# Kernel tuning notes

Measured on AMD Instinct MI355X. Metric: run time of the kernel, lower is better.

The kernel has to match this reference:

```python
import jax, jax.numpy as jnp
import numpy as np

N_LEVELS = 16
N_FEATS = 2
LOG2_T = 19
TABLE_SIZE = 2 ** LOG2_T
BASE_RES = 16
PER_LEVEL_SCALE = 1.3819
N_PTS = 524288
# per-level grid resolutions (static)
RESOLUTIONS = np.floor(BASE_RES * PER_LEVEL_SCALE ** np.arange(N_LEVELS)).astype(np.float32)
# NGP spatial hash primes for 2D
PRIME0 = np.uint32(1)
PRIME1 = np.uint32(2654435761)
# corner offsets for bilinear interp: (0,0),(0,1),(1,0),(1,1)
CORNER_OFFS = np.array([[0, 0], [0, 1], [1, 0], [1, 1]], dtype=np.uint32)


def setup_inputs() -> dict:
    key = jax.random.key(0)
    k1, k2 = jax.random.split(key)
    pts = jax.random.uniform(k1, (N_PTS, 3), dtype=jnp.float32)  # coords in [0,1]
    # 3 planes x L levels x T entries x F features, small init like NGP (1e-4)
    tables = jax.random.normal(k2, (3, N_LEVELS, TABLE_SIZE, N_FEATS), dtype=jnp.float32) * 1e-4
    return {"pts": pts, "tables": tables}


def _encode_plane(coords, table):
    # coords: [N,2] in [0,1]; table: [L,T,F]
    L, T, F = table.shape
    res = jnp.asarray(RESOLUTIONS)  # [L]
    scaled = coords[None, :, :] * res[:, None, None]  # [L,N,2]
    x0 = jnp.floor(scaled)
    frac = scaled - x0  # [L,N,2]
    x0u = x0.astype(jnp.uint32)
    offs = jnp.asarray(CORNER_OFFS)  # [4,2]
    corners = x0u[:, :, None, :] + offs[None, None, :, :]  # [L,N,4,2]
    # NGP spatial hash with uint32 wraparound, then mod table size
    h = (corners[..., 0] * PRIME0) ^ (corners[..., 1] * PRIME1)  # [L,N,4] uint32
    idx = (h % jnp.uint32(T)).astype(jnp.int32)  # [L,N,4]
    feats = table[jnp.arange(L)[:, None, None], idx]  # [L,N,4,F]
    # bilinear weights: product over dims of frac (offset=1) or 1-frac (offset=0)
    fo = offs.astype(coords.dtype)  # [4,2]
    w = jnp.prod(jnp.where(fo[None, None] > 0, frac[:, :, None, :], 1.0 - frac[:, :, None, :]), axis=-1)  # [L,N,4]
    out = jnp.einsum('lnc,lncf->lnf', w, feats)  # [L,N,F]
    return out.transpose(1, 0, 2).reshape(coords.shape[0], L * F)  # [N, L*F]


def reference(pts, tables):
    # coordinate-pair planes: combinations of (0,1,2) taken 2 at a time
    coo_combs = [(0, 1), (0, 2), (1, 2)]
    interp_space = 1.0
    for ci, comb in enumerate(coo_combs):
        interp_space = interp_space * _encode_plane(pts[:, list(comb)], tables[ci])
    return interp_space  # [N, 32]
```

## Files before the change

kernel.cpp:

```cpp
#include <hip/hip_runtime.h>
#include <stdint.h>


#define NPTS   524288u
#define TSIZE  524288u
#define TMASK  0x7FFFFu
#define PRIME1 2654435761u

__constant__ float c_res[16] = {
    16.f, 22.f, 30.f, 42.f, 58.f, 80.f, 111.f, 153.f,
    212.f, 294.f, 406.f, 561.f, 775.f, 1072.f, 1481.f, 2047.f
};
__constant__ int c_resi[6] = {16, 22, 30, 42, 58, 80};

__constant__ uint8_t c_hmap[32] = {
    15, 31, 47, 14, 30, 46, 13, 29,
    45, 28, 44, 12, 11, 27, 43, 10,
    26, 42,  9, 25, 41,  8, 24, 40,
     7, 23, 39,  6, 22, 38, 255, 255
};

__global__ __launch_bounds__(512) void kplane_lds(
    const float* __restrict__ pts,
    const float2* __restrict__ tab,
    float2* __restrict__ ws)
{
    __shared__ float2 sm[6561];
    const uint32_t b     = blockIdx.x;
    const uint32_t gidx  = b >> 6;
    const uint32_t chunk = b & 63u;
    const uint32_t plane = gidx / 6u;
    const uint32_t lvl   = gidx - plane * 6u;
    const uint32_t g     = plane * 16u + lvl;
    const uint32_t R     = (uint32_t)c_resi[lvl] + 1u;
    const uint32_t E     = R * R;
    const float    res   = c_res[lvl];
    const uint32_t base  = g * TSIZE;
    const uint32_t t     = threadIdx.x;

    for (uint32_t i = t; i < E; i += 512u) {
        const uint32_t cx = i / R;
        const uint32_t cy = i - cx * R;
        sm[i] = tab[base + ((cx ^ (cy * PRIME1)) & TMASK)];
    }
    __syncthreads();

    const uint32_t c0  = (plane == 2u) ? 1u : 0u;
    const uint32_t c1  = (plane == 0u) ? 1u : 2u;
    const uint32_t pt0 = chunk * 8192u + t;

#pragma unroll 4
    for (uint32_t k = 0; k < 16u; ++k) {
        const uint32_t pt = pt0 + k * 512u;
        const float s0 = pts[pt * 3u + c0] * res;
        const float s1 = pts[pt * 3u + c1] * res;
        const float f0 = floorf(s0);
        const float f1 = floorf(s1);
        const float r0 = s0 - f0;
        const float r1 = s1 - f1;
        const uint32_t ci = (uint32_t)f0 * R + (uint32_t)f1;
        const float2 q00 = sm[ci];
        const float2 q01 = sm[ci + 1u];
        const float2 q10 = sm[ci + R];
        const float2 q11 = sm[ci + R + 1u];
        const float w00 = (1.f - r0) * (1.f - r1);
        const float w01 = (1.f - r0) * r1;
        const float w10 = r0 * (1.f - r1);
        const float w11 = r0 * r1;
        ws[g * NPTS + pt] = make_float2(
            w00 * q00.x + w01 * q01.x + w10 * q10.x + w11 * q11.x,
            w00 * q00.y + w01 * q01.y + w10 * q10.y + w11 * q11.y);
    }
}

__global__ __launch_bounds__(256) void kplane_hi(
    const float* __restrict__ pts,
    const float2* __restrict__ tab,
    float2* __restrict__ ws)
{
    const uint32_t b     = blockIdx.x;
    const uint32_t xcd   = b & 7u;
    const uint32_t s     = b >> 3;
    const uint32_t phase = s >> 10;
    const uint32_t chunk = s & 1023u;
    const uint32_t g     = c_hmap[phase * 8u + xcd];
    if (g == 255u) return;
    const uint32_t plane = g >> 4;
    const uint32_t lvl   = g & 15u;
    const float    res   = c_res[lvl];
    const uint32_t c0    = (plane == 2u) ? 1u : 0u;
    const uint32_t c1    = (plane == 0u) ? 1u : 2u;
    const uint32_t base  = g * TSIZE;
    const float4* __restrict__ tab4 = (const float4*)tab;
    const uint32_t b4    = g * (TSIZE / 2u);
    const uint32_t pt0   = chunk * 512u + threadIdx.x;

    float4 P0[2], P1[2];
    float2 Q0[2], Q1[2];
    float  r0[2], r1[2];
    uint32_t sel0[2], sel1[2], oddm[2];

#pragma unroll
    for (int k = 0; k < 2; ++k) {
        const uint32_t pt = pt0 + (uint32_t)k * 256u;
        const float s0 = pts[pt * 3u + c0] * res;
        const float s1 = pts[pt * 3u + c1] * res;
        const float f0 = floorf(s0);
        const float f1 = floorf(s1);
        r0[k] = s0 - f0;
        r1[k] = s1 - f1;
        const uint32_t u0  = (uint32_t)f0;
        const uint32_t hy0 = (uint32_t)f1 * PRIME1;
        const uint32_t hy1 = hy0 + PRIME1;
        const uint32_t i00 = ( u0        ^ hy0) & TMASK;
        const uint32_t i01 = ( u0        ^ hy1) & TMASK;
        const uint32_t i10 = ((u0 + 1u)  ^ hy0) & TMASK;
        const uint32_t i11 = ((u0 + 1u)  ^ hy1) & TMASK;
        sel0[k] = i00 & 1u;
        sel1[k] = i01 & 1u;
        oddm[k] = u0 & 1u;
        P0[k] = tab4[b4 + (i00 >> 1)];
        P1[k] = tab4[b4 + (i01 >> 1)];
        Q0[k] = make_float2(0.f, 0.f);
        Q1[k] = make_float2(0.f, 0.f);
        if (oddm[k]) {
            Q0[k] = tab[base + i10];
            Q1[k] = tab[base + i11];
        }
    }
#pragma unroll
    for (int k = 0; k < 2; ++k) {
        const uint32_t pt = pt0 + (uint32_t)k * 256u;
        const float2 lo0 = make_float2(P0[k].x, P0[k].y);
        const float2 hi0 = make_float2(P0[k].z, P0[k].w);
        const float2 lo1 = make_float2(P1[k].x, P1[k].y);
        const float2 hi1 = make_float2(P1[k].z, P1[k].w);
        const float2 t00 = sel0[k] ? hi0 : lo0;
        const float2 t01 = sel1[k] ? hi1 : lo1;
        const float2 t10 = oddm[k] ? Q0[k] : (sel0[k] ? lo0 : hi0);
        const float2 t11 = oddm[k] ? Q1[k] : (sel1[k] ? lo1 : hi1);
        const float w00 = (1.f - r0[k]) * (1.f - r1[k]);
        const float w01 = (1.f - r0[k]) * r1[k];
        const float w10 = r0[k] * (1.f - r1[k]);
        const float w11 = r0[k] * r1[k];
        ws[g * NPTS + pt] = make_float2(
            w00 * t00.x + w01 * t01.x + w10 * t10.x + w11 * t11.x,
            w00 * t00.y + w01 * t01.y + w10 * t10.y + w11 * t11.y);
    }
}

__global__ __launch_bounds__(256) void kplane_combine(
    const float2* __restrict__ ws,
    float2* __restrict__ out)
{
    __shared__ float2 tile[16][65];
    const uint32_t pt0 = blockIdx.x * 64u;
    const uint32_t t   = threadIdx.x;
    const uint32_t lr  = t >> 6;
    const uint32_t ptl = t & 63u;

#pragma unroll
    for (int k = 0; k < 4; ++k) {
        const uint32_t lvl = (uint32_t)k * 4u + lr;
        const float2 a = ws[( 0u + lvl) * NPTS + pt0 + ptl];
        const float2 b = ws[(16u + lvl) * NPTS + pt0 + ptl];
        const float2 c = ws[(32u + lvl) * NPTS + pt0 + ptl];
        tile[lvl][ptl] = make_float2(a.x * b.x * c.x, a.y * b.y * c.y);
    }
    __syncthreads();
#pragma unroll
    for (int k = 0; k < 4; ++k) {
        const uint32_t e      = t + (uint32_t)k * 256u;
        const uint32_t out_lv = e & 15u;
        const uint32_t out_pt = e >> 4;
        out[(pt0 + out_pt) * 16u + out_lv] = tile[out_lv][out_pt];
    }
}

template <int P, bool FIRST>
__global__ __launch_bounds__(256) void kplane_pass(
    const float* __restrict__ pts,
    const float2* __restrict__ tab,
    float2* __restrict__ ws)
{
    const uint32_t b     = blockIdx.x;
    const uint32_t xcd   = b & 7u;
    const uint32_t s     = b >> 3;
    const uint32_t gi    = s >> 11;
    const uint32_t chunk = s & 2047u;
    const uint32_t lvl   = gi * 8u + xcd;
    const uint32_t pt    = chunk * 256u + threadIdx.x;

    constexpr int c0 = (P == 2) ? 1 : 0;
    constexpr int c1 = (P == 0) ? 1 : 2;

    const float a0  = pts[pt * 3u + c0];
    const float a1  = pts[pt * 3u + c1];
    const float res = c_res[lvl];

    const float s0 = a0 * res;
    const float s1 = a1 * res;
    const float f0 = floorf(s0);
    const float f1 = floorf(s1);
    const float r0 = s0 - f0;
    const float r1 = s1 - f1;
    const uint32_t u0 = (uint32_t)f0;
    const uint32_t hy0  = (uint32_t)f1 * PRIME1;
    const uint32_t hy1  = hy0 + PRIME1;
    const uint32_t base = ((uint32_t)P * 16u + lvl) * TSIZE;

    const float2 t00 = tab[base + (( u0       ^ hy0) & TMASK)];
    const float2 t01 = tab[base + (( u0       ^ hy1) & TMASK)];
    const float2 t10 = tab[base + (((u0 + 1u) ^ hy0) & TMASK)];
    const float2 t11 = tab[base + (((u0 + 1u) ^ hy1) & TMASK)];

    const float w00 = (1.f - r0) * (1.f - r1);
    const float w01 = (1.f - r0) * r1;
    const float w10 = r0 * (1.f - r1);
    const float w11 = r0 * r1;

    const float e0 = w00 * t00.x + w01 * t01.x + w10 * t10.x + w11 * t11.x;
    const float e1 = w00 * t00.y + w01 * t01.y + w10 * t10.y + w11 * t11.y;

    const uint32_t widx = lvl * NPTS + pt;
    if (FIRST) {
        ws[widx] = make_float2(e0, e1);
    } else {
        const float2 prev = ws[widx];
        ws[widx] = make_float2(prev.x * e0, prev.y * e1);
    }
}

__global__ __launch_bounds__(256) void kplane_transpose(
    const float2* __restrict__ ws, float2* __restrict__ out)
{
    const uint32_t tid = blockIdx.x * 256u + threadIdx.x;
    const uint32_t lvl = tid & 15u;
    const uint32_t pt  = tid >> 4;
    out[tid] = ws[lvl * NPTS + pt];
}

extern "C" void kernel_launch(void* const* d_in, const int* in_sizes, int n_in,
                              void* d_out, int out_size, void* d_ws, size_t ws_size,
                              hipStream_t stream) {
    const float*  pts = (const float*)d_in[0];
    const float2* tab = (const float2*)d_in[1];
    float2*       out = (float2*)d_out;

    const size_t wsA = (size_t)48 * NPTS * sizeof(float2);
    const size_t wsB = (size_t)16 * NPTS * sizeof(float2);
    dim3 block256(256u), block512(512u);

    if (ws_size >= wsA) {
        float2* ws = (float2*)d_ws;
        dim3 hgrid(4u * 8u * 1024u);
        hipLaunchKernelGGL(kplane_hi, hgrid, block256, 0, stream, pts, tab, ws);
        dim3 lgrid(18u * 64u);
        hipLaunchKernelGGL(kplane_lds, lgrid, block512, 0, stream, pts, tab, ws);
        dim3 cgrid(NPTS / 64u);
        hipLaunchKernelGGL(kplane_combine, cgrid, block256, 0, stream, ws, out);
    } else if (ws_size >= wsB) {
        float2* ws = (float2*)d_ws;
        dim3 grid(16u * (NPTS / 256u));
        hipLaunchKernelGGL((kplane_pass<0, true >), grid, block256, 0, stream, pts, tab, ws);
        hipLaunchKernelGGL((kplane_pass<1, false>), grid, block256, 0, stream, pts, tab, ws);
        hipLaunchKernelGGL((kplane_pass<2, false>), grid, block256, 0, stream, pts, tab, ws);
        dim3 tgrid((NPTS * 16u) / 256u);
        hipLaunchKernelGGL(kplane_transpose, tgrid, block256, 0, stream, ws, out);
    }
}
```

Measured before the change: 288.2 us.

## Stage levels 6-7 hash tables in LDS via row-split blocks, rebalance hashed kernel

Adds a kplane_mid kernel that handles levels 6 and 7 for all three planes. It splits each level's dense grid into row bands small enough to fit in LDS, and every block filters points to its band before doing bilinear lookups from shared memory. kplane_hi now covers only levels 8-15, with a simpler per-XCD level mapping and four points per thread. This is meant to move gathers for the mid levels from global memory to LDS and to give more latency hiding per thread. The cost is that every mid block reads all points in its chunk and discards most of them, and there is one extra kernel launch.

```diff
diff --git a/kernel.cpp b/kernel.cpp
--- a/kernel.cpp
+++ b/kernel.cpp
@@ -13,12 +13,8 @@
 };
 __constant__ int c_resi[6] = {16, 22, 30, 42, 58, 80};
 
-__constant__ uint8_t c_hmap[32] = {
-    15, 31, 47, 14, 30, 46, 13, 29,
-    45, 28, 44, 12, 11, 27, 43, 10,
-    26, 42,  9, 25, 41,  8, 24, 40,
-     7, 23, 39,  6, 22, 38, 255, 255
-};
+__constant__ uint16_t c_mid_lo[6]  = {0, 56, 0, 39, 78, 117};
+__constant__ uint16_t c_mid_hiX[6] = {56, 112, 39, 78, 117, 154};
 
 __global__ __launch_bounds__(512) void kplane_lds(
     const float* __restrict__ pts,
@@ -73,6 +69,67 @@
     }
 }
 
+__global__ __launch_bounds__(512) void kplane_mid(
+    const float* __restrict__ pts,
+    const float2* __restrict__ tab,
+    float2* __restrict__ ws)
+{
+    __shared__ float2 sm[6400];
+    const uint32_t b     = blockIdx.x;
+    const uint32_t sg    = b >> 5;
+    const uint32_t chunk = b & 31u;
+    const uint32_t plane = sg / 6u;
+    const uint32_t local = sg - plane * 6u;
+    const uint32_t lvl   = (local < 2u) ? 6u : 7u;
+    const uint32_t g     = plane * 16u + lvl;
+    const uint32_t R     = (lvl == 6u) ? 112u : 154u;
+    const uint32_t lo    = c_mid_lo[local];
+    const uint32_t hiX   = c_mid_hiX[local];
+    const uint32_t nrows = ((hiX < R ? hiX : R - 1u) - lo) + 1u;
+    const uint32_t E     = nrows * R;
+    const float    res   = c_res[lvl];
+    const uint32_t base  = g * TSIZE;
+    const uint32_t t     = threadIdx.x;
+
+    for (uint32_t i = t; i < E; i += 512u) {
+        const uint32_t rr = i / R;
+        const uint32_t cy = i - rr * R;
+        const uint32_t cx = lo + rr;
+        sm[i] = tab[base + ((cx ^ (cy * PRIME1)) & TMASK)];
+    }
+    __syncthreads();
+
+    const uint32_t c0  = (plane == 2u) ? 1u : 0u;
+    const uint32_t c1  = (plane == 0u) ? 1u : 2u;
+    const uint32_t pt0 = chunk * 16384u + t;
+
+#pragma unroll 4
+    for (uint32_t k = 0; k < 32u; ++k) {
+        const uint32_t pt = pt0 + k * 512u;
+        const float s0 = pts[pt * 3u + c0] * res;
+        const float s1 = pts[pt * 3u + c1] * res;
+        const float f0 = floorf(s0);
+        const float f1 = floorf(s1);
+        const uint32_t u0 = (uint32_t)f0;
+        if (u0 >= lo && u0 < hiX) {
+            const float r0 = s0 - f0;
+            const float r1 = s1 - f1;
+            const uint32_t ci = (u0 - lo) * R + (uint32_t)f1;
+            const float2 q00 = sm[ci];
+            const float2 q01 = sm[ci + 1u];
+            const float2 q10 = sm[ci + R];
+            const float2 q11 = sm[ci + R + 1u];
+            const float w00 = (1.f - r0) * (1.f - r1);
+            const float w01 = (1.f - r0) * r1;
+            const float w10 = r0 * (1.f - r1);
+            const float w11 = r0 * r1;
+            ws[g * NPTS + pt] = make_float2(
+                w00 * q00.x + w01 * q01.x + w10 * q10.x + w11 * q11.x,
+                w00 * q00.y + w01 * q01.y + w10 * q10.y + w11 * q11.y);
+        }
+    }
+}
+
 __global__ __launch_bounds__(256) void kplane_hi(
     const float* __restrict__ pts,
     const float2* __restrict__ tab,
@@ -81,27 +138,26 @@
     const uint32_t b     = blockIdx.x;
     const uint32_t xcd   = b & 7u;
     const uint32_t s     = b >> 3;
-    const uint32_t phase = s >> 10;
-    const uint32_t chunk = s & 1023u;
-    const uint32_t g     = c_hmap[phase * 8u + xcd];
-    if (g == 255u) return;
-    const uint32_t plane = g >> 4;
-    const uint32_t lvl   = g & 15u;
+    const uint32_t phase = s >> 9;
+    const uint32_t chunk = s & 511u;
+    const uint32_t plane = phase;
+    const uint32_t lvl   = 8u + ((xcd + 3u * phase) & 7u);
+    const uint32_t g     = plane * 16u + lvl;
     const float    res   = c_res[lvl];
     const uint32_t c0    = (plane == 2u) ? 1u : 0u;
     const uint32_t c1    = (plane == 0u) ? 1u : 2u;
     const uint32_t base  = g * TSIZE;
     const float4* __restrict__ tab4 = (const float4*)tab;
     const uint32_t b4    = g * (TSIZE / 2u);
-    const uint32_t pt0   = chunk * 512u + threadIdx.x;
-
-    float4 P0[2], P1[2];
-    float2 Q0[2], Q1[2];
-    float  r0[2], r1[2];
-    uint32_t sel0[2], sel1[2], oddm[2];
+    const uint32_t pt0   = chunk * 1024u + threadIdx.x;
+
+    float4 P0[4], P1[4];
+    float2 Q0[4], Q1[4];
+    float  r0[4], r1[4];
+    uint32_t sel0[4], sel1[4], oddm[4];
 
 #pragma unroll
-    for (int k = 0; k < 2; ++k) {
+    for (int k = 0; k < 4; ++k) {
         const uint32_t pt = pt0 + (uint32_t)k * 256u;
         const float s0 = pts[pt * 3u + c0] * res;
         const float s1 = pts[pt * 3u + c1] * res;
@@ -129,7 +185,7 @@
         }
     }
 #pragma unroll
-    for (int k = 0; k < 2; ++k) {
+    for (int k = 0; k < 4; ++k) {
         const uint32_t pt = pt0 + (uint32_t)k * 256u;
         const float2 lo0 = make_float2(P0[k].x, P0[k].y);
         const float2 hi0 = make_float2(P0[k].z, P0[k].w);
@@ -253,8 +309,10 @@
 
     if (ws_size >= wsA) {
         float2* ws = (float2*)d_ws;
-        dim3 hgrid(4u * 8u * 1024u);
+        dim3 hgrid(3u * 8u * 512u);
         hipLaunchKernelGGL(kplane_hi, hgrid, block256, 0, stream, pts, tab, ws);
+        dim3 mgrid(18u * 32u);
+        hipLaunchKernelGGL(kplane_mid, mgrid, block512, 0, stream, pts, tab, ws);
         dim3 lgrid(18u * 64u);
         hipLaunchKernelGGL(kplane_lds, lgrid, block512, 0, stream, pts, tab, ws);
         dim3 cgrid(NPTS / 64u);
```

Result: faster. 277.2 us (-3.8%).
